# Kernel tuning notes

Measured on AMD Instinct MI355X. Metric: run time of the kernel, lower is better.

Reference implementation:

```python
import jax, jax.numpy as jnp
import numpy as np

NUM_ROUTERS = 8
K = 2
IN_DIM = 384
HID = 64
TEMP = 1.0
AUX_COEF = 0.05
EPS = 1e-12


def _l2norm(v, axis=-1):
    n = jnp.sqrt(jnp.sum(v * v, axis=axis, keepdims=True))
    return v / jnp.maximum(n, EPS)


def setup_inputs() -> dict:
    key = jax.random.key(0)
    ks = jax.random.split(key, 10)
    B, E = 8192, 1024
    s = 1.0 / np.sqrt(IN_DIM)
    return {
        "x": jax.random.normal(ks[0], (B, IN_DIM), jnp.float32),
        "reasoning_embeddings": jax.random.normal(ks[1], (E, IN_DIM), jnp.float32),
        "random_num": jax.random.uniform(ks[2], (B, 1), jnp.float32),
        "gate_w": jax.random.normal(ks[3], (IN_DIM, NUM_ROUTERS), jnp.float32) * s,
        "gate_b": jnp.zeros((NUM_ROUTERS,), jnp.float32),
        "Uw": jax.random.normal(ks[4], (NUM_ROUTERS, IN_DIM, HID), jnp.float32) * s,
        "Ub": jnp.zeros((NUM_ROUTERS, HID), jnp.float32),
        "Vw": jax.random.normal(ks[5], (NUM_ROUTERS, IN_DIM, HID), jnp.float32) * s,
        "Vb": jnp.zeros((NUM_ROUTERS, HID), jnp.float32),
    }


def reference(x, reasoning_embeddings, random_num, gate_w, gate_b, Uw, Ub, Vw, Vb):
    B = x.shape[0]
    # gate
    logits = x @ gate_w + gate_b                              # [B, R]
    probs = jax.nn.softmax(logits, axis=-1)
    topk_vals, topk_idxs = jax.lax.top_k(logits, K)           # [B, K]
    topk_mask = jax.nn.one_hot(topk_idxs, NUM_ROUTERS).sum(axis=1)  # [B, R]
    aux_loss = NUM_ROUTERS * (probs.mean(0) * topk_mask.mean(0)).sum() * AUX_COEF

    # all routers, batched (replaces the per-(i,j) python loop)
    xu = _l2norm(jnp.einsum("bd,rdh->rbh", x, Uw) + Ub[:, None, :])          # [R, B, H]
    ev = _l2norm(jnp.einsum("ed,rdh->reh", reasoning_embeddings, Vw) + Vb[:, None, :])  # [R, E, H]
    scores = jnp.einsum("rbh,reh->rbe", xu, ev)               # [R, B, E]
    all_out = jax.nn.softmax(scores / TEMP, axis=-1)          # [R, B, E]

    # gather top-k experts per sample
    all_out_b = jnp.transpose(all_out, (1, 0, 2))             # [B, R, E]
    router_outputs = jnp.take_along_axis(all_out_b, topk_idxs[:, :, None], axis=1)  # [B, K, E]

    gate_weights = jax.nn.softmax(topk_vals, axis=-1)[:, :, None]  # [B, K, 1]
    rea_probs = jnp.sum(router_outputs * gate_weights, axis=1)     # [B, E]

    # categorical sampling via inverse-CDF
    scores_cumsum = jnp.cumsum(rea_probs, axis=1)
    selected_index = jnp.argmax((scores_cumsum > random_num).astype(jnp.float32), axis=1)  # [B]
    log_probs = jnp.log(rea_probs[jnp.arange(B), selected_index])[:, None]  # [B, 1]
    return selected_index, log_probs, aux_loss
```

## Files before the change

kernel.cpp:

```cpp
#include <hip/hip_runtime.h>
#include <math.h>

#define B 8192
#define E 1024
#define D 384
#define H 64
#define R 8
#define NCHUNK 16
#define CHUNK_E 64

#define WS_COUNTS   0u
#define WS_CURSORS  32u
#define WS_PS       64u
#define WS_OFFSETS  96u
#define WS_TOP2     256u
#define WS_GW       65792u
#define WS_LIST     131328u
#define WS_EVN      196864u
#define WS_XUN      2294016u
#define WS_C        6488320u
#define WS_POSMAP   7536896u

__global__ __launch_bounds__(256) void k_gate(
    const float* __restrict__ x, const float* __restrict__ gate_w,
    const float* __restrict__ gate_b, int2* __restrict__ top2,
    float2* __restrict__ gwv, int* __restrict__ counts, float* __restrict__ ps)
{
  __shared__ __align__(16) float gwT[R * 388];
  __shared__ float psl[R];
  __shared__ int   cl[R];
  int tid = threadIdx.x;
  for (int idx = tid; idx < D * R; idx += 256) {
    int k = idx >> 3, r = idx & 7;
    gwT[r * 388 + k] = gate_w[idx];
  }
  if (tid < R) { psl[tid] = 0.f; cl[tid] = 0; }
  __syncthreads();

  int l = tid & 63;
  int r = tid & 7;
  int b = blockIdx.x * 32 + (tid >> 3);
  float acc = gate_b[r];
  const float4* x4 = (const float4*)(x + (size_t)b * D);
  const float*  gr = gwT + r * 388;
#pragma unroll 4
  for (int q = 0; q < 96; ++q) {
    float4 xv = x4[q];
    float4 gv = *(const float4*)&gr[q * 4];
    acc = fmaf(xv.x, gv.x, acc);
    acc = fmaf(xv.y, gv.y, acc);
    acc = fmaf(xv.z, gv.z, acc);
    acc = fmaf(xv.w, gv.w, acc);
  }
  float lv[R];
#pragma unroll
  for (int rr = 0; rr < R; ++rr) lv[rr] = __shfl(acc, (l & ~7) + rr);
  int i0 = 0; float v0 = lv[0];
#pragma unroll
  for (int rr = 1; rr < R; ++rr) if (lv[rr] > v0) { v0 = lv[rr]; i0 = rr; }
  int i1 = (i0 == 0) ? 1 : 0; float v1 = lv[i1];
#pragma unroll
  for (int rr = 0; rr < R; ++rr)
    if (rr != i0 && lv[rr] > v1) { v1 = lv[rr]; i1 = rr; }
  float se = 0.f;
#pragma unroll
  for (int rr = 0; rr < R; ++rr) se += expf(lv[rr] - v0);
  float p = expf(acc - v0) / se;
  if (r == 0) {
    float e10 = expf(v1 - v0);
    top2[b] = make_int2(i0, i1);
    gwv[b]  = make_float2(1.f / (1.f + e10), e10 / (1.f + e10));
  }
  float pa = p;
  int   ca = (r == i0 ? 1 : 0) + (r == i1 ? 1 : 0);
#pragma unroll
  for (int m = 8; m < 64; m <<= 1) {
    pa += __shfl_xor(pa, m);
    ca += __shfl_xor(ca, m);
  }
  if (l < 8) { atomicAdd(&psl[r], pa); atomicAdd(&cl[r], ca); }
  __syncthreads();
  if (tid < R) { atomicAdd(&ps[tid], psl[tid]); atomicAdd(&counts[tid], cl[tid]); }
}

__global__ void k_combine(const int* __restrict__ counts, const float* __restrict__ ps,
                          int* __restrict__ offsets, float* __restrict__ out_aux)
{
  if (threadIdx.x == 0 && blockIdx.x == 0) {
    int off = 0; float s = 0.f;
    for (int r = 0; r < R; ++r) {
      offsets[r] = off; off += counts[r];
      s += (ps[r] / (float)B) * ((float)counts[r] / (float)B);
    }
    out_aux[0] = (float)R * s * 0.05f;
  }
}

__global__ __launch_bounds__(256) void k_scatter(
    const int2* __restrict__ top2, const int* __restrict__ offsets,
    int* __restrict__ cursors, int* __restrict__ list, int2* __restrict__ posmap)
{
  __shared__ int lc[R];
  __shared__ int lbase[R];
  int tid = threadIdx.x;
  if (tid < R) lc[tid] = 0;
  __syncthreads();
  int b = min(blockIdx.x * 256 + tid, B - 1);
  int2 t = top2[b];
  t.x &= 7; t.y &= 7;
  int p0 = atomicAdd(&lc[t.x], 1);
  int p1 = atomicAdd(&lc[t.y], 1);
  __syncthreads();
  if (tid < R) lbase[tid] = atomicAdd(&cursors[tid], lc[tid]);
  __syncthreads();
  int i0 = min(offsets[t.x] + lbase[t.x] + p0, 2 * B - 1);
  int i1 = min(offsets[t.y] + lbase[t.y] + p1, 2 * B - 1);
  list[i0] = b * 2 + 0;
  list[i1] = b * 2 + 1;
  posmap[b] = make_int2(i0, i1);
}

__global__ __launch_bounds__(256) void k_evn(
    const float* __restrict__ re, const float* __restrict__ Vw,
    const float* __restrict__ Vb, float* __restrict__ evnT)
{
  __shared__ __align__(16) float At[64 * 64];
  __shared__ __align__(16) float Wt[64 * 64];
  int tid = threadIdx.x;
  int rg0 = blockIdx.x * 64;
  int r = rg0 >> 10;
  int e0 = rg0 & 1023;
  int tc = tid & 15, tr = tid >> 4;
  float4 vb = *(const float4*)(Vb + r * H + tc * 4);
  float acc[4][4];
#pragma unroll
  for (int i = 0; i < 4; ++i) { acc[i][0] = vb.x; acc[i][1] = vb.y; acc[i][2] = vb.z; acc[i][3] = vb.w; }

  int arow = tid >> 2, ac = tid & 3;
  const float4* Asrc = (const float4*)re + (size_t)(e0 + arow) * 96;
  const float4* Wsrc = (const float4*)Vw + (size_t)r * 6144;

  for (int kt = 0; kt < 6; ++kt) {
    __syncthreads();
#pragma unroll
    for (int i = 0; i < 4; ++i) {
      float4 v = Asrc[kt * 16 + ac + 4 * i];
      int colb = (ac + 4 * i) * 4;
#pragma unroll
      for (int m = 0; m < 4; ++m) {
        int col = colb + m;
        At[col * 64 + (arow ^ ((col & 15) << 2))] = ((const float*)&v)[m];
      }
    }
#pragma unroll
    for (int i = 0; i < 4; ++i) {
      int idx = tid + 256 * i;
      *(float4*)&Wt[idx * 4] = Wsrc[kt * 1024 + idx];
    }
    __syncthreads();
    for (int k = 0; k < 64; ++k) {
      float4 a4 = *(const float4*)&At[k * 64 + ((tr * 4) ^ ((k & 15) << 2))];
      float4 w4 = *(const float4*)&Wt[k * 64 + tc * 4];
      const float* ap = (const float*)&a4;
      const float* wp = (const float*)&w4;
#pragma unroll
      for (int i = 0; i < 4; ++i)
#pragma unroll
        for (int j = 0; j < 4; ++j) acc[i][j] = fmaf(ap[i], wp[j], acc[i][j]);
    }
  }
  float rn[4];
#pragma unroll
  for (int i = 0; i < 4; ++i) {
    float ss = 0.f;
#pragma unroll
    for (int j = 0; j < 4; ++j) ss = fmaf(acc[i][j], acc[i][j], ss);
#pragma unroll
    for (int m = 1; m < 16; m <<= 1) ss += __shfl_xor(ss, m);
    rn[i] = 1.f / fmaxf(sqrtf(ss), 1e-12f);
  }
#pragma unroll
  for (int j = 0; j < 4; ++j) {
    float4 o;
    o.x = acc[0][j] * rn[0]; o.y = acc[1][j] * rn[1];
    o.z = acc[2][j] * rn[2]; o.w = acc[3][j] * rn[3];
    *(float4*)(evnT + ((size_t)(r * 64 + tc * 4 + j) * 1024) + e0 + tr * 4) = o;
  }
}

__global__ __launch_bounds__(256) void k_xun(
    const float* __restrict__ x, const float* __restrict__ Uw,
    const float* __restrict__ Ub, const int* __restrict__ list,
    const int* __restrict__ counts, const int* __restrict__ offsets,
    float* __restrict__ xunP)
{
  int r = blockIdx.x >> 7;
  int tile = blockIdx.x & 127;
  int cnt = min(counts[r], B);
  if (cnt <= 0 || tile * 64 >= cnt) return;
  int n = min(64, cnt - tile * 64);
  int base = offsets[r] + tile * 64;

  __shared__ __align__(16) float At[64 * 64];
  __shared__ __align__(16) float Wt[64 * 64];
  int tid = threadIdx.x;
  int tc = tid & 15, tr = tid >> 4;
  float4 ub = *(const float4*)(Ub + r * H + tc * 4);
  float acc[4][4];
#pragma unroll
  for (int i = 0; i < 4; ++i) { acc[i][0] = ub.x; acc[i][1] = ub.y; acc[i][2] = ub.z; acc[i][3] = ub.w; }

  int arow = tid >> 2, ac = tid & 3;
  int ga = list[min(base + min(arow, n - 1), 2 * B - 1)] & (2 * B - 1);
  const float4* Asrc = (const float4*)x + (size_t)(ga >> 1) * 96;
  const float4* Wsrc = (const float4*)Uw + (size_t)r * 6144;

  for (int kt = 0; kt < 6; ++kt) {
    __syncthreads();
#pragma unroll
    for (int i = 0; i < 4; ++i) {
      float4 v = Asrc[kt * 16 + ac + 4 * i];
      int colb = (ac + 4 * i) * 4;
#pragma unroll
      for (int m = 0; m < 4; ++m) {
        int col = colb + m;
        At[col * 64 + (arow ^ ((col & 15) << 2))] = ((const float*)&v)[m];
      }
    }
#pragma unroll
    for (int i = 0; i < 4; ++i) {
      int idx = tid + 256 * i;
      *(float4*)&Wt[idx * 4] = Wsrc[kt * 1024 + idx];
    }
    __syncthreads();
    for (int k = 0; k < 64; ++k) {
      float4 a4 = *(const float4*)&At[k * 64 + ((tr * 4) ^ ((k & 15) << 2))];
      float4 w4 = *(const float4*)&Wt[k * 64 + tc * 4];
      const float* ap = (const float*)&a4;
      const float* wp = (const float*)&w4;
#pragma unroll
      for (int i = 0; i < 4; ++i)
#pragma unroll
        for (int j = 0; j < 4; ++j) acc[i][j] = fmaf(ap[i], wp[j], acc[i][j]);
    }
  }
#pragma unroll
  for (int i = 0; i < 4; ++i) {
    int row = tr * 4 + i;
    float ss = 0.f;
#pragma unroll
    for (int j = 0; j < 4; ++j) ss = fmaf(acc[i][j], acc[i][j], ss);
#pragma unroll
    for (int m = 1; m < 16; m <<= 1) ss += __shfl_xor(ss, m);
    float rn = 1.f / fmaxf(sqrtf(ss), 1e-12f);
    if (row < n) {
      float4 o; o.x = acc[i][0] * rn; o.y = acc[i][1] * rn; o.z = acc[i][2] * rn; o.w = acc[i][3] * rn;
      *(float4*)(xunP + (size_t)(base + row) * H + tc * 4) = o;
    }
  }
}

__global__ __launch_bounds__(256) void k_pass1(
    const float* __restrict__ evnT, const float* __restrict__ xunP,
    const int* __restrict__ counts, const int* __restrict__ offsets,
    float* __restrict__ C)
{
  int bid = blockIdx.x;
  int et    = bid & 15;
  int stile = (bid >> 4) & 63;
  int r     = bid >> 10;
  int cnt = min(counts[r], B);
  if (cnt <= 0 || stile * 128 >= cnt) return;
  int off = offsets[r] + stile * 128;
  int n = min(128, cnt - stile * 128);
  int ebase = et * 64;

  __shared__ __align__(16) float Xt[64 * 128];
  __shared__ __align__(16) float Et[64 * 64];
  int tid = threadIdx.x;

  {
    int row = tid >> 1;
    int rc  = min(row, n - 1);
    const float4* src = (const float4*)(xunP + (size_t)(off + rc) * H);
    int hq0 = (tid & 1) * 8;
#pragma unroll
    for (int q = 0; q < 8; ++q) {
      float4 v = src[hq0 + q];
      int h = (hq0 + q) * 4;
      Xt[(h + 0) * 128 + row] = v.x;
      Xt[(h + 1) * 128 + row] = v.y;
      Xt[(h + 2) * 128 + row] = v.z;
      Xt[(h + 3) * 128 + row] = v.w;
    }
  }
  {
#pragma unroll
    for (int q = 0; q < 4; ++q) {
      int idx = tid + 256 * q;
      int h = idx >> 4, e4 = idx & 15;
      float4 v = *(const float4*)(evnT + (size_t)(r * 64 + h) * 1024 + ebase + e4 * 4);
      *(float4*)&Et[h * 64 + e4 * 4] = v;
    }
  }
  __syncthreads();

  int sg = tid >> 4, egr = tid & 15;
  float acc[8][4];
#pragma unroll
  for (int i = 0; i < 8; ++i)
#pragma unroll
    for (int j = 0; j < 4; ++j) acc[i][j] = 0.f;

#pragma unroll 4
  for (int k = 0; k < 64; ++k) {
    float4 xa = *(const float4*)&Xt[k * 128 + sg * 8];
    float4 xb = *(const float4*)&Xt[k * 128 + sg * 8 + 4];
    float4 ev = *(const float4*)&Et[k * 64 + egr * 4];
    const float* ep = (const float*)&ev;
    const float* pa = (const float*)&xa;
    const float* pb = (const float*)&xb;
#pragma unroll
    for (int i = 0; i < 4; ++i)
#pragma unroll
      for (int j = 0; j < 4; ++j) {
        acc[i][j]     = fmaf(pa[i], ep[j], acc[i][j]);
        acc[i + 4][j] = fmaf(pb[i], ep[j], acc[i + 4][j]);
      }
  }

#pragma unroll
  for (int i = 0; i < 8; ++i) {
    float v = expf(acc[i][0]) + expf(acc[i][1]) + expf(acc[i][2]) + expf(acc[i][3]);
#pragma unroll
    for (int m = 1; m < 16; m <<= 1) v += __shfl_xor(v, m);
    int s = sg * 8 + i;
    if (egr == 0 && s < n) C[(size_t)(off + s) * NCHUNK + et] = v;
  }
}

__global__ __launch_bounds__(256) void k_pass2(
    const float* __restrict__ evnT, const float* __restrict__ xunP,
    const float* __restrict__ C, const int2* __restrict__ top2,
    const int2* __restrict__ posmap, const float2* __restrict__ gwv,
    const float* __restrict__ rnd, float* __restrict__ out)
{
  int tid = threadIdx.x;
  int lane = tid & 63;
  int b = blockIdx.x * 4 + (tid >> 6);
  if (b >= B) return;
  int2 t2 = top2[b];
  t2.x &= 7; t2.y &= 7;
  int2 pm = posmap[b];
  pm.x &= (2 * B - 1); pm.y &= (2 * B - 1);
  float2 gw = gwv[b];
  float rv = rnd[b];

  const float4* C04 = (const float4*)(C + (size_t)pm.x * NCHUNK);
  const float4* C14 = (const float4*)(C + (size_t)pm.y * NCHUNK);
  float c0[NCHUNK], c1[NCHUNK];
#pragma unroll
  for (int q = 0; q < 4; ++q) {
    float4 v0 = C04[q], v1 = C14[q];
    c0[q*4+0]=v0.x; c0[q*4+1]=v0.y; c0[q*4+2]=v0.z; c0[q*4+3]=v0.w;
    c1[q*4+0]=v1.x; c1[q*4+1]=v1.y; c1[q*4+2]=v1.z; c1[q*4+3]=v1.w;
  }
  float S0 = 0.f, S1 = 0.f;
#pragma unroll
  for (int j = 0; j < NCHUNK; ++j) { S0 += c0[j]; S1 += c1[j]; }
  float a0 = gw.x / S0, a1 = gw.y / S1;
  int cstar = -1; float prefix = 0.f; float run = 0.f;
#pragma unroll
  for (int j = 0; j < NCHUNK; ++j) {
    float nrun = run + (c0[j] * a0 + c1[j] * a1);
    if (cstar < 0 && nrun > rv) { cstar = j; prefix = run; }
    run = nrun;
  }
  float rtgt = rv;
  if (cstar < 0) { cstar = 0; prefix = 0.f; rtgt = -1.0f; }

  float xu0 = xunP[(size_t)pm.x * H + lane];
  float xu1 = xunP[(size_t)pm.y * H + lane];
  const float* E0 = evnT + (size_t)t2.x * 64 * 1024 + cstar * CHUNK_E + lane;
  const float* E1 = evnT + (size_t)t2.y * 64 * 1024 + cstar * CHUNK_E + lane;
  float d0 = 0.f, d1 = 0.f;
#pragma unroll 16
  for (int h = 0; h < 64; ++h) {
    float w0 = __shfl(xu0, h);
    float w1 = __shfl(xu1, h);
    d0 = fmaf(E0[(size_t)h * 1024], w0, d0);
    d1 = fmaf(E1[(size_t)h * 1024], w1, d1);
  }
  float rea = expf(d0) * a0 + expf(d1) * a1;
  float sc = rea;
#pragma unroll
  for (int d = 1; d < 64; d <<= 1) {
    float o = __shfl_up(sc, d);
    if (lane >= d) sc += o;
  }
  float cum = prefix + sc;
  unsigned long long m2 = __ballot(cum > rtgt);
  int estar = (m2 == 0ull) ? 63 : (int)__builtin_ctzll(m2);
  float p = __shfl(rea, estar);
  if (lane == 0) {
    int sel = cstar * CHUNK_E + estar;
    out[b]     = (float)sel;
    out[B + b] = logf(p);
  }
}

extern "C" void kernel_launch(void* const* d_in, const int* in_sizes, int n_in,
                              void* d_out, int out_size, void* d_ws, size_t ws_size,
                              hipStream_t stream)
{
  (void)in_sizes; (void)n_in; (void)out_size; (void)ws_size;
  const float* x      = (const float*)d_in[0];
  const float* re     = (const float*)d_in[1];
  const float* rnd    = (const float*)d_in[2];
  const float* gate_w = (const float*)d_in[3];
  const float* gate_b = (const float*)d_in[4];
  const float* Uw     = (const float*)d_in[5];
  const float* Ub     = (const float*)d_in[6];
  const float* Vw     = (const float*)d_in[7];
  const float* Vb     = (const float*)d_in[8];
  char* ws = (char*)d_ws;
  int*    counts  = (int*)(ws + WS_COUNTS);
  int*    cursors = (int*)(ws + WS_CURSORS);
  float*  ps      = (float*)(ws + WS_PS);
  int*    offsets = (int*)(ws + WS_OFFSETS);
  int2*   top2    = (int2*)(ws + WS_TOP2);
  float2* gwv     = (float2*)(ws + WS_GW);
  int*    list    = (int*)(ws + WS_LIST);
  float*  evnT    = (float*)(ws + WS_EVN);
  float*  xunP    = (float*)(ws + WS_XUN);
  float*  Cc      = (float*)(ws + WS_C);
  int2*   posmap  = (int2*)(ws + WS_POSMAP);
  float* out = (float*)d_out;

  hipMemsetAsync(ws, 0, 256, stream);
  k_gate   <<<256,  256, 0, stream>>>(x, gate_w, gate_b, top2, gwv, counts, ps);
  k_combine<<<1,    64,  0, stream>>>(counts, ps, offsets, out + 2 * B);
  k_scatter<<<32,   256, 0, stream>>>(top2, offsets, cursors, list, posmap);
  k_evn    <<<128,  256, 0, stream>>>(re, Vw, Vb, evnT);
  k_xun    <<<1024, 256, 0, stream>>>(x, Uw, Ub, list, counts, offsets, xunP);
  k_pass1  <<<8192, 256, 0, stream>>>(evnT, xunP, counts, offsets, Cc);
  k_pass2  <<<2048, 256, 0, stream>>>(evnT, xunP, Cc, top2, posmap, gwv, rnd, out);
}
```

Measured before the change: 213.0 us.

## Fuse combine into scatter and merge projection kernels into one launch

```diff
diff --git a/kernel.cpp b/kernel.cpp
--- a/kernel.cpp
+++ b/kernel.cpp
@@ -12,7 +12,6 @@
 #define WS_COUNTS   0u
 #define WS_CURSORS  32u
 #define WS_PS       64u
-#define WS_OFFSETS  96u
 #define WS_TOP2     256u
 #define WS_GW       65792u
 #define WS_LIST     131328u
@@ -83,27 +82,21 @@
   if (tid < R) { atomicAdd(&ps[tid], psl[tid]); atomicAdd(&counts[tid], cl[tid]); }
 }
 
-__global__ void k_combine(const int* __restrict__ counts, const float* __restrict__ ps,
-                          int* __restrict__ offsets, float* __restrict__ out_aux)
-{
-  if (threadIdx.x == 0 && blockIdx.x == 0) {
-    int off = 0; float s = 0.f;
-    for (int r = 0; r < R; ++r) {
-      offsets[r] = off; off += counts[r];
-      s += (ps[r] / (float)B) * ((float)counts[r] / (float)B);
-    }
-    out_aux[0] = (float)R * s * 0.05f;
-  }
-}
-
 __global__ __launch_bounds__(256) void k_scatter(
-    const int2* __restrict__ top2, const int* __restrict__ offsets,
-    int* __restrict__ cursors, int* __restrict__ list, int2* __restrict__ posmap)
+    const int2* __restrict__ top2, const int* __restrict__ counts,
+    const float* __restrict__ ps, int* __restrict__ cursors,
+    int* __restrict__ list, int2* __restrict__ posmap, float* __restrict__ out_aux)
 {
   __shared__ int lc[R];
   __shared__ int lbase[R];
+  __shared__ int offs[R];
   int tid = threadIdx.x;
-  if (tid < R) lc[tid] = 0;
+  if (tid < R) { lc[tid] = 0; offs[tid] = min(counts[tid], B); }
+  __syncthreads();
+  if (tid == 0) {
+    int o = 0;
+    for (int r2 = 0; r2 < R; ++r2) { int c = offs[r2]; offs[r2] = o; o += c; }
+  }
   __syncthreads();
   int b = min(blockIdx.x * 256 + tid, B - 1);
   int2 t = top2[b];
@@ -113,54 +106,92 @@
   __syncthreads();
   if (tid < R) lbase[tid] = atomicAdd(&cursors[tid], lc[tid]);
   __syncthreads();
-  int i0 = min(offsets[t.x] + lbase[t.x] + p0, 2 * B - 1);
-  int i1 = min(offsets[t.y] + lbase[t.y] + p1, 2 * B - 1);
+  int i0 = min(offs[t.x] + lbase[t.x] + p0, 2 * B - 1);
+  int i1 = min(offs[t.y] + lbase[t.y] + p1, 2 * B - 1);
   list[i0] = b * 2 + 0;
   list[i1] = b * 2 + 1;
   posmap[b] = make_int2(i0, i1);
-}
-
-__global__ __launch_bounds__(256) void k_evn(
-    const float* __restrict__ re, const float* __restrict__ Vw,
-    const float* __restrict__ Vb, float* __restrict__ evnT)
-{
-  __shared__ __align__(16) float At[64 * 64];
+  if (blockIdx.x == 0 && tid == 0) {
+    float s = 0.f;
+    for (int r2 = 0; r2 < R; ++r2)
+      s += (ps[r2] / (float)B) * ((float)min(counts[r2], B) / (float)B);
+    out_aux[0] = (float)R * s * 0.05f;
+  }
+}
+
+__global__ __launch_bounds__(128) void k_proj(
+    const float* __restrict__ re, const float* __restrict__ x,
+    const float* __restrict__ Vw, const float* __restrict__ Vb,
+    const float* __restrict__ Uw, const float* __restrict__ Ub,
+    const int* __restrict__ list, const int* __restrict__ counts,
+    float* __restrict__ evnT, float* __restrict__ xunP)
+{
+  __shared__ __align__(16) float At[64 * 32];
   __shared__ __align__(16) float Wt[64 * 64];
+  __shared__ int cntL[R];
   int tid = threadIdx.x;
-  int rg0 = blockIdx.x * 64;
-  int r = rg0 >> 10;
-  int e0 = rg0 & 1023;
-  int tc = tid & 15, tr = tid >> 4;
-  float4 vb = *(const float4*)(Vb + r * H + tc * 4);
+  int bid = blockIdx.x;
+  if (tid < R) cntL[tid] = min(counts[tid], B);
+  __syncthreads();
+
+  bool isE = (bid < 256);
+  int r, row0, n, base = 0;
+  const float* Wsrc; const float* bias;
+  if (isE) {
+    r = bid >> 5; row0 = (bid & 31) * 32; n = 32;
+    Wsrc = Vw + (size_t)r * D * H; bias = Vb + r * H;
+  } else {
+    int idx = bid - 256;
+    r = idx >> 8; row0 = (idx & 255) * 32;
+    int cnt = cntL[r];
+    if (row0 >= cnt) return;
+    n = min(32, cnt - row0);
+    for (int rr = 0; rr < r; ++rr) base += cntL[rr];
+    base += row0;
+    Wsrc = Uw + (size_t)r * D * H; bias = Ub + r * H;
+  }
+
+  int rowS = tid & 31, kq = tid >> 5;
+  const float4* Arow;
+  if (isE) {
+    Arow = (const float4*)re + (size_t)(row0 + rowS) * 96;
+  } else {
+    int g = list[min(base + min(rowS, n - 1), 2 * B - 1)] & (2 * B - 1);
+    Arow = (const float4*)x + (size_t)(g >> 1) * 96;
+  }
+  const float4* W4 = (const float4*)Wsrc;
+
+  int rg = tid >> 4;
+  int hg = tid & 15;
+  float4 bv = *(const float4*)(bias + hg * 4);
   float acc[4][4];
 #pragma unroll
-  for (int i = 0; i < 4; ++i) { acc[i][0] = vb.x; acc[i][1] = vb.y; acc[i][2] = vb.z; acc[i][3] = vb.w; }
-
-  int arow = tid >> 2, ac = tid & 3;
-  const float4* Asrc = (const float4*)re + (size_t)(e0 + arow) * 96;
-  const float4* Wsrc = (const float4*)Vw + (size_t)r * 6144;
+  for (int i = 0; i < 4; ++i) {
+    acc[i][0] = bv.x; acc[i][1] = bv.y; acc[i][2] = bv.z; acc[i][3] = bv.w;
+  }
 
   for (int kt = 0; kt < 6; ++kt) {
     __syncthreads();
 #pragma unroll
-    for (int i = 0; i < 4; ++i) {
-      float4 v = Asrc[kt * 16 + ac + 4 * i];
-      int colb = (ac + 4 * i) * 4;
-#pragma unroll
-      for (int m = 0; m < 4; ++m) {
-        int col = colb + m;
-        At[col * 64 + (arow ^ ((col & 15) << 2))] = ((const float*)&v)[m];
-      }
-    }
-#pragma unroll
-    for (int i = 0; i < 4; ++i) {
-      int idx = tid + 256 * i;
-      *(float4*)&Wt[idx * 4] = Wsrc[kt * 1024 + idx];
+    for (int q = 0; q < 4; ++q) {
+      float4 v = Arow[kt * 16 + kq + 4 * q];
+      int kb = (kq + 4 * q) * 4;
+      At[(kb + 0) * 32 + rowS] = v.x;
+      At[(kb + 1) * 32 + rowS] = v.y;
+      At[(kb + 2) * 32 + rowS] = v.z;
+      At[(kb + 3) * 32 + rowS] = v.w;
+    }
+#pragma unroll
+    for (int q = 0; q < 8; ++q) {
+      int idx2 = tid + 128 * q;
+      int k = idx2 >> 4, h4 = idx2 & 15;
+      *(float4*)&Wt[k * 64 + h4 * 4] = W4[(size_t)(kt * 64 + k) * 16 + h4];
     }
     __syncthreads();
+#pragma unroll 8
     for (int k = 0; k < 64; ++k) {
-      float4 a4 = *(const float4*)&At[k * 64 + ((tr * 4) ^ ((k & 15) << 2))];
-      float4 w4 = *(const float4*)&Wt[k * 64 + tc * 4];
+      float4 a4 = *(const float4*)&At[k * 32 + rg * 4];
+      float4 w4 = *(const float4*)&Wt[k * 64 + hg * 4];
       const float* ap = (const float*)&a4;
       const float* wp = (const float*)&w4;
 #pragma unroll
@@ -169,6 +200,7 @@
         for (int j = 0; j < 4; ++j) acc[i][j] = fmaf(ap[i], wp[j], acc[i][j]);
     }
   }
+
   float rn[4];
 #pragma unroll
   for (int i = 0; i < 4; ++i) {
@@ -179,105 +211,51 @@
     for (int m = 1; m < 16; m <<= 1) ss += __shfl_xor(ss, m);
     rn[i] = 1.f / fmaxf(sqrtf(ss), 1e-12f);
   }
-#pragma unroll
-  for (int j = 0; j < 4; ++j) {
-    float4 o;
-    o.x = acc[0][j] * rn[0]; o.y = acc[1][j] * rn[1];
-    o.z = acc[2][j] * rn[2]; o.w = acc[3][j] * rn[3];
-    *(float4*)(evnT + ((size_t)(r * 64 + tc * 4 + j) * 1024) + e0 + tr * 4) = o;
-  }
-}
-
-__global__ __launch_bounds__(256) void k_xun(
-    const float* __restrict__ x, const float* __restrict__ Uw,
-    const float* __restrict__ Ub, const int* __restrict__ list,
-    const int* __restrict__ counts, const int* __restrict__ offsets,
-    float* __restrict__ xunP)
-{
-  int r = blockIdx.x >> 7;
-  int tile = blockIdx.x & 127;
-  int cnt = min(counts[r], B);
-  if (cnt <= 0 || tile * 64 >= cnt) return;
-  int n = min(64, cnt - tile * 64);
-  int base = offsets[r] + tile * 64;
-
-  __shared__ __align__(16) float At[64 * 64];
-  __shared__ __align__(16) float Wt[64 * 64];
-  int tid = threadIdx.x;
-  int tc = tid & 15, tr = tid >> 4;
-  float4 ub = *(const float4*)(Ub + r * H + tc * 4);
-  float acc[4][4];
-#pragma unroll
-  for (int i = 0; i < 4; ++i) { acc[i][0] = ub.x; acc[i][1] = ub.y; acc[i][2] = ub.z; acc[i][3] = ub.w; }
-
-  int arow = tid >> 2, ac = tid & 3;
-  int ga = list[min(base + min(arow, n - 1), 2 * B - 1)] & (2 * B - 1);
-  const float4* Asrc = (const float4*)x + (size_t)(ga >> 1) * 96;
-  const float4* Wsrc = (const float4*)Uw + (size_t)r * 6144;
-
-  for (int kt = 0; kt < 6; ++kt) {
-    __syncthreads();
+
+  if (isE) {
+#pragma unroll
+    for (int j = 0; j < 4; ++j) {
+      float4 o;
+      o.x = acc[0][j] * rn[0]; o.y = acc[1][j] * rn[1];
+      o.z = acc[2][j] * rn[2]; o.w = acc[3][j] * rn[3];
+      *(float4*)(evnT + (size_t)(r * 64 + hg * 4 + j) * 1024 + row0 + rg * 4) = o;
+    }
+  } else {
 #pragma unroll
     for (int i = 0; i < 4; ++i) {
-      float4 v = Asrc[kt * 16 + ac + 4 * i];
-      int colb = (ac + 4 * i) * 4;
-#pragma unroll
-      for (int m = 0; m < 4; ++m) {
-        int col = colb + m;
-        At[col * 64 + (arow ^ ((col & 15) << 2))] = ((const float*)&v)[m];
+      int row = rg * 4 + i;
+      if (row < n) {
+        float4 o;
+        o.x = acc[i][0] * rn[i]; o.y = acc[i][1] * rn[i];
+        o.z = acc[i][2] * rn[i]; o.w = acc[i][3] * rn[i];
+        *(float4*)(xunP + (size_t)(base + row) * H + hg * 4) = o;
       }
-    }
-#pragma unroll
-    for (int i = 0; i < 4; ++i) {
-      int idx = tid + 256 * i;
-      *(float4*)&Wt[idx * 4] = Wsrc[kt * 1024 + idx];
-    }
-    __syncthreads();
-    for (int k = 0; k < 64; ++k) {
-      float4 a4 = *(const float4*)&At[k * 64 + ((tr * 4) ^ ((k & 15) << 2))];
-      float4 w4 = *(const float4*)&Wt[k * 64 + tc * 4];
-      const float* ap = (const float*)&a4;
-      const float* wp = (const float*)&w4;
-#pragma unroll
-      for (int i = 0; i < 4; ++i)
-#pragma unroll
-        for (int j = 0; j < 4; ++j) acc[i][j] = fmaf(ap[i], wp[j], acc[i][j]);
-    }
-  }
-#pragma unroll
-  for (int i = 0; i < 4; ++i) {
-    int row = tr * 4 + i;
-    float ss = 0.f;
-#pragma unroll
-    for (int j = 0; j < 4; ++j) ss = fmaf(acc[i][j], acc[i][j], ss);
-#pragma unroll
-    for (int m = 1; m < 16; m <<= 1) ss += __shfl_xor(ss, m);
-    float rn = 1.f / fmaxf(sqrtf(ss), 1e-12f);
-    if (row < n) {
-      float4 o; o.x = acc[i][0] * rn; o.y = acc[i][1] * rn; o.z = acc[i][2] * rn; o.w = acc[i][3] * rn;
-      *(float4*)(xunP + (size_t)(base + row) * H + tc * 4) = o;
     }
   }
 }
 
 __global__ __launch_bounds__(256) void k_pass1(
     const float* __restrict__ evnT, const float* __restrict__ xunP,
-    const int* __restrict__ counts, const int* __restrict__ offsets,
-    float* __restrict__ C)
-{
+    const int* __restrict__ counts, float* __restrict__ C)
+{
+  __shared__ __align__(16) float Xt[64 * 128];
+  __shared__ __align__(16) float Et[64 * 64];
+  __shared__ int cntL[R];
+  int tid = threadIdx.x;
+  if (tid < R) cntL[tid] = min(counts[tid], B);
+  __syncthreads();
+
   int bid = blockIdx.x;
   int et    = bid & 15;
   int stile = (bid >> 4) & 63;
   int r     = bid >> 10;
-  int cnt = min(counts[r], B);
+  int cnt = cntL[r];
   if (cnt <= 0 || stile * 128 >= cnt) return;
-  int off = offsets[r] + stile * 128;
+  int off = 0;
+  for (int rr = 0; rr < r; ++rr) off += cntL[rr];
+  off += stile * 128;
   int n = min(128, cnt - stile * 128);
   int ebase = et * 64;
-
-  __shared__ __align__(16) float Xt[64 * 128];
-  __shared__ __align__(16) float Et[64 * 64];
-  int tid = threadIdx.x;
 
   {
     int row = tid >> 1;
@@ -427,7 +405,6 @@
   int*    counts  = (int*)(ws + WS_COUNTS);
   int*    cursors = (int*)(ws + WS_CURSORS);
   float*  ps      = (float*)(ws + WS_PS);
-  int*    offsets = (int*)(ws + WS_OFFSETS);
   int2*   top2    = (int2*)(ws + WS_TOP2);
   float2* gwv     = (float2*)(ws + WS_GW);
   int*    list    = (int*)(ws + WS_LIST);
@@ -439,10 +416,8 @@
 
   hipMemsetAsync(ws, 0, 256, stream);
   k_gate   <<<256,  256, 0, stream>>>(x, gate_w, gate_b, top2, gwv, counts, ps);
-  k_combine<<<1,    64,  0, stream>>>(counts, ps, offsets, out + 2 * B);
-  k_scatter<<<32,   256, 0, stream>>>(top2, offsets, cursors, list, posmap);
-  k_evn    <<<128,  256, 0, stream>>>(re, Vw, Vb, evnT);
-  k_xun    <<<1024, 256, 0, stream>>>(x, Uw, Ub, list, counts, offsets, xunP);
-  k_pass1  <<<8192, 256, 0, stream>>>(evnT, xunP, counts, offsets, Cc);
+  k_scatter<<<32,   256, 0, stream>>>(top2, counts, ps, cursors, list, posmap, out + 2 * B);
+  k_proj   <<<2304, 128, 0, stream>>>(re, x, Vw, Vb, Uw, Ub, list, counts, evnT, xunP);
+  k_pass1  <<<8192, 256, 0, stream>>>(evnT, xunP, counts, Cc);
   k_pass2  <<<2048, 256, 0, stream>>>(evnT, xunP, Cc, top2, posmap, gwv, rnd, out);
 }
```

New measurement: 184.7 us. 13.3% less time.
